# Performance work log

Hardware: AMD Instinct MI355X
Metric: run time of the kernel (lower is better)

## Reference

```python
import jax, jax.numpy as jnp
import numpy as np

D_MODEL = 1024
N_HEADS = 16
D_HEAD = D_MODEL // N_HEADS


def setup_inputs() -> dict:
    key = jax.random.key(0)
    ks = jax.random.split(key, 5)
    scale = 1.0 / np.sqrt(D_MODEL)
    return {
        "x": jax.random.normal(ks[0], (2, 2048, D_MODEL), dtype=jnp.float32),
        "W_q": jax.random.normal(ks[1], (D_MODEL, D_MODEL), dtype=jnp.float32) * scale,
        "W_k": jax.random.normal(ks[2], (D_MODEL, D_MODEL), dtype=jnp.float32) * scale,
        "W_v": jax.random.normal(ks[3], (D_MODEL, D_MODEL), dtype=jnp.float32) * scale,
        "W_o": jax.random.normal(ks[4], (D_MODEL, D_MODEL), dtype=jnp.float32) * scale,
    }


def reference(x, W_q, W_k, W_v, W_o):
    B, S, _ = x.shape
    # nn.Linear computes x @ W.T; weights stored [out, in]
    def proj(W):
        y = jnp.einsum("bsd,ed->bse", x, W)
        return y.reshape(B, S, N_HEADS, D_HEAD).transpose(0, 2, 1, 3)  # [B,H,S,Dh]

    q, k, v = proj(W_q), proj(W_k), proj(W_v)
    scores = jnp.einsum("bhqd,bhkd->bhqk", q, k) / jnp.sqrt(jnp.float32(D_HEAD))
    causal = jnp.triu(jnp.ones((S, S), dtype=bool), k=1)
    scores = jnp.where(causal, -jnp.inf, scores)
    attn = jax.nn.softmax(scores, axis=-1)
    out = jnp.einsum("bhqk,bhkd->bhqd", attn, v)  # [B,H,S,Dh]
    out = out.transpose(0, 2, 1, 3).reshape(B, S, D_MODEL)
    return jnp.einsum("bsd,ed->bse", out, W_o)
```

## Files before the change

kernel.cpp:

```cpp
#include <hip/hip_runtime.h>


#define DMODEL 1024
#define NHEADS 16
#define DHEAD  64
#define SEQ    2048
#define BATCH  2
#define MROWS  (BATCH * SEQ)

typedef __bf16 bf16x8 __attribute__((ext_vector_type(8)));
typedef __bf16 bf16x4 __attribute__((ext_vector_type(4)));
typedef float  f32x4  __attribute__((ext_vector_type(4)));

__device__ __forceinline__ f32x4 mfma16(bf16x8 a, bf16x8 b, f32x4 c) {
    return __builtin_amdgcn_mfma_f32_16x16x32_bf16(a, b, c, 0, 0, 0);
}

__device__ __forceinline__ bf16x8 ld8(const float* p) {
    const f32x4 a0 = *(const f32x4*)p;
    const f32x4 a1 = *(const f32x4*)(p + 4);
    bf16x8 v;
    v[0] = (__bf16)a0[0]; v[1] = (__bf16)a0[1];
    v[2] = (__bf16)a0[2]; v[3] = (__bf16)a0[3];
    v[4] = (__bf16)a1[0]; v[5] = (__bf16)a1[1];
    v[6] = (__bf16)a1[2]; v[7] = (__bf16)a1[3];
    return v;
}

__device__ __forceinline__ void gll16(const __bf16* g, __bf16* l) {
    __builtin_amdgcn_global_load_lds(
        (const __attribute__((address_space(1))) void*)g,
        (__attribute__((address_space(3))) void*)l,
        16, 0, 0);
}

__global__ __launch_bounds__(256) void cvt_kernel(const float* __restrict__ x,
                                                  const float* __restrict__ Wq,
                                                  const float* __restrict__ Wk,
                                                  const float* __restrict__ Wv,
                                                  const float* __restrict__ Wo,
                                                  __bf16* __restrict__ xb,
                                                  __bf16* __restrict__ wcat) {
    const int y = blockIdx.y;
    const float* src;
    __bf16* dst;
    int nchunks;
    if (y == 0) { src = x; dst = xb; nchunks = (MROWS * DMODEL) / 8; }
    else {
        src = (y == 1) ? Wq : (y == 2) ? Wk : (y == 3) ? Wv : Wo;
        dst = wcat + (size_t)(y - 1) * DMODEL * DMODEL;
        nchunks = (DMODEL * DMODEL) / 8;
    }
    const int c = blockIdx.x * 256 + threadIdx.x;
    if (c < nchunks) *(bf16x8*)(dst + (size_t)c * 8) = ld8(src + (size_t)c * 8);
}

template <typename TC>
__device__ __forceinline__ void gemm_bb_body(const __bf16* __restrict__ A,
                                             const __bf16* __restrict__ W,
                                             TC* __restrict__ C,
                                             int m0, int n0) {
    constexpr int K = DMODEL;
    __shared__ __align__(16) __bf16 As[128][32];
    __shared__ __align__(16) __bf16 Bs[128][32];

    const int tid  = threadIdx.x;
    const int lane = tid & 63;
    const int wave = tid >> 6;
    const int quad = lane >> 4;
    const int l16  = lane & 15;
    const int wm   = wave & 1;
    const int wn   = wave >> 1;

    const int srow = lane >> 2;
    const int scol = (lane & 3) * 8;

    const __bf16* a0p = A + (size_t)(m0 + wave * 16 + srow) * K + scol;
    const __bf16* a1p = A + (size_t)(m0 + 64 + wave * 16 + srow) * K + scol;
    const __bf16* b0p = W + (size_t)(n0 + wave * 16 + srow) * K + scol;
    const __bf16* b1p = W + (size_t)(n0 + 64 + wave * 16 + srow) * K + scol;

    f32x4 acc[4][4] = {};

    for (int k0 = 0; k0 < K; k0 += 32) {
        __syncthreads();
        gll16(a0p + k0, &As[wave * 16][0]);
        gll16(a1p + k0, &As[64 + wave * 16][0]);
        gll16(b0p + k0, &Bs[wave * 16][0]);
        gll16(b1p + k0, &Bs[64 + wave * 16][0]);
        __syncthreads();

        bf16x8 af[4], bfr[4];
#pragma unroll
        for (int i = 0; i < 4; ++i) {
            af[i]  = *(const bf16x8*)(&As[wm * 64 + i * 16 + l16][quad * 8]);
            bfr[i] = *(const bf16x8*)(&Bs[wn * 64 + i * 16 + l16][quad * 8]);
        }
#pragma unroll
        for (int mi = 0; mi < 4; ++mi)
#pragma unroll
            for (int ni = 0; ni < 4; ++ni)
                acc[mi][ni] = mfma16(af[mi], bfr[ni], acc[mi][ni]);
    }

#pragma unroll
    for (int mi = 0; mi < 4; ++mi)
#pragma unroll
        for (int ni = 0; ni < 4; ++ni)
#pragma unroll
            for (int r = 0; r < 4; ++r) {
                int row = m0 + wm * 64 + mi * 16 + quad * 4 + r;
                int col = n0 + wn * 64 + ni * 16 + l16;
                C[(size_t)row * DMODEL + col] = (TC)acc[mi][ni][r];
            }
}

__global__ __launch_bounds__(256) void qkv_kernel(const __bf16* __restrict__ X,
                                                  const __bf16* __restrict__ wcat,
                                                  __bf16* __restrict__ QKV) {
    const __bf16* W = wcat + (size_t)blockIdx.z * DMODEL * DMODEL;
    __bf16*       Y = QKV + (size_t)blockIdx.z * MROWS * DMODEL;
    gemm_bb_body<__bf16>(X, W, Y, blockIdx.y * 128, blockIdx.x * 128);
}

__global__ __launch_bounds__(256) void out_gemm_kernel(const __bf16* __restrict__ A,
                                                       const __bf16* __restrict__ W,
                                                       float* __restrict__ C) {
    gemm_bb_body<float>(A, W, C, blockIdx.y * 128, blockIdx.x * 128);
}

__global__ __launch_bounds__(128) void attn_kernel(const __bf16* __restrict__ Q,
                                                   const __bf16* __restrict__ Kg,
                                                   const __bf16* __restrict__ Vg,
                                                   __bf16* __restrict__ O) {
    const int pr = blockIdx.x;
    const int bh = blockIdx.y;
    const int b = bh >> 4, h = bh & 15;
    const size_t base = (size_t)b * SEQ * DMODEL + (size_t)h * DHEAD;

    const int tid  = threadIdx.x;
    const int lane = tid & 63;
    const int wave = tid >> 6;
    const int quad = lane >> 4;
    const int l16  = lane & 15;

    __shared__ __align__(16) __bf16 Ks[32][80];
    __shared__ __align__(16) __bf16 Vt[64][40];
    __shared__ __align__(16) __bf16 Ps[2][16][40];

    const int ldr = tid >> 2;
    const int c0  = (tid & 3) * 16;
    const int vcol = (((ldr >> 3) ^ (c0 >> 4)) << 3) | (ldr & 7);

#pragma unroll
    for (int sel = 0; sel < 2; ++sel) {
        const int qt = sel ? (63 - pr) : pr;
        const int qrow = qt * 32 + wave * 16 + l16;

        const bf16x8 qf0 = *(const bf16x8*)(Q + base + (size_t)qrow * DMODEL + quad * 8);
        const bf16x8 qf1 = *(const bf16x8*)(Q + base + (size_t)qrow * DMODEL + 32 + quad * 8);

        f32x4 oacc[4] = {};
        float m_i = -1e30f, l_i = 0.f;

        const int ktiles = qt + 1;

        const __bf16* kp = Kg + base + (size_t)ldr * DMODEL + c0;
        const __bf16* vp = Vg + base + (size_t)ldr * DMODEL + c0;
        bf16x8 pk0 = *(const bf16x8*)(kp);
        bf16x8 pk1 = *(const bf16x8*)(kp + 8);
        bf16x8 pv0 = *(const bf16x8*)(vp);
        bf16x8 pv1 = *(const bf16x8*)(vp + 8);

        for (int kt = 0; kt < ktiles; ++kt) {
            *(bf16x8*)(&Ks[ldr][c0])     = pk0;
            *(bf16x8*)(&Ks[ldr][c0 + 8]) = pk1;
#pragma unroll
            for (int i = 0; i < 8; ++i) {
                Vt[c0 + i][vcol]     = pv0[i];
                Vt[c0 + 8 + i][vcol] = pv1[i];
            }
            __syncthreads();

            if (kt + 1 < ktiles) {
                const __bf16* kp2 = Kg + base + (size_t)((kt + 1) * 32 + ldr) * DMODEL + c0;
                const __bf16* vp2 = Vg + base + (size_t)((kt + 1) * 32 + ldr) * DMODEL + c0;
                pk0 = *(const bf16x8*)(kp2);
                pk1 = *(const bf16x8*)(kp2 + 8);
                pv0 = *(const bf16x8*)(vp2);
                pv1 = *(const bf16x8*)(vp2 + 8);
            }

            const int k0 = kt * 32;

            const bf16x8 kf00 = *(const bf16x8*)(&Ks[l16][quad * 8]);
            const bf16x8 kf01 = *(const bf16x8*)(&Ks[l16][32 + quad * 8]);
            const bf16x8 kf10 = *(const bf16x8*)(&Ks[16 + l16][quad * 8]);
            const bf16x8 kf11 = *(const bf16x8*)(&Ks[16 + l16][32 + quad * 8]);
            f32x4 s0 = {}, s1 = {};
            s0 = mfma16(kf00, qf0, s0); s0 = mfma16(kf01, qf1, s0);
            s1 = mfma16(kf10, qf0, s1); s1 = mfma16(kf11, qf1, s1);

            float sc[2][4];
            bool  ok[2][4];
            float mx = -1e30f;
#pragma unroll
            for (int hh = 0; hh < 2; ++hh)
#pragma unroll
                for (int r = 0; r < 4; ++r) {
                    const int kk = k0 + hh * 16 + quad * 4 + r;
                    const float v = (hh ? s1[r] : s0[r]) * 0.125f;
                    sc[hh][r] = v;
                    ok[hh][r] = (kk <= qrow);
                    mx = fmaxf(mx, ok[hh][r] ? v : -1e30f);
                }
            mx = fmaxf(mx, __shfl_xor(mx, 16));
            mx = fmaxf(mx, __shfl_xor(mx, 32));
            const float mnew  = fmaxf(m_i, mx);
            const float alpha = __expf(m_i - mnew);
            m_i = mnew;

            float p[2][4];
            float rs = 0.f;
#pragma unroll
            for (int hh = 0; hh < 2; ++hh)
#pragma unroll
                for (int r = 0; r < 4; ++r) {
                    p[hh][r] = ok[hh][r] ? __expf(sc[hh][r] - mnew) : 0.f;
                    rs += p[hh][r];
                }
            rs += __shfl_xor(rs, 16);
            rs += __shfl_xor(rs, 32);
            l_i = l_i * alpha + rs;

            bf16x4 w0, w1;
#pragma unroll
            for (int r = 0; r < 4; ++r) { w0[r] = (__bf16)p[0][r]; w1[r] = (__bf16)p[1][r]; }
            *(bf16x4*)(&Ps[wave][l16][quad * 4])      = w0;
            *(bf16x4*)(&Ps[wave][l16][16 + quad * 4]) = w1;

            const bf16x8 pf = *(const bf16x8*)(&Ps[wave][l16][quad * 8]);
#pragma unroll
            for (int f = 0; f < 4; ++f) {
                const bf16x8 vf = *(const bf16x8*)(&Vt[f * 16 + l16][(quad ^ f) * 8]);
                oacc[f] = mfma16(vf, pf, oacc[f] * alpha);
            }
            __syncthreads();
        }

        const float inv = (l_i > 0.f) ? (1.f / l_i) : 0.f;
#pragma unroll
        for (int f = 0; f < 4; ++f) {
            bf16x4 o;
#pragma unroll
            for (int r = 0; r < 4; ++r) o[r] = (__bf16)(oacc[f][r] * inv);
            *(bf16x4*)(O + base + (size_t)qrow * DMODEL + f * 16 + quad * 4) = o;
        }
    }
}

extern "C" void kernel_launch(void* const* d_in, const int* in_sizes, int n_in,
                              void* d_out, int out_size, void* d_ws, size_t ws_size,
                              hipStream_t stream) {
    const float* x  = (const float*)d_in[0];
    const float* Wq = (const float*)d_in[1];
    const float* Wk = (const float*)d_in[2];
    const float* Wv = (const float*)d_in[3];
    const float* Wo = (const float*)d_in[4];
    float* out = (float*)d_out;

    const size_t tm = (size_t)MROWS * DMODEL;
    const size_t tw = (size_t)DMODEL * DMODEL;
    __bf16* xb   = (__bf16*)d_ws;
    __bf16* wcat = xb + tm;
    __bf16* QKV  = wcat + 4 * tw;
    __bf16* Q = QKV;
    __bf16* K = QKV + tm;
    __bf16* V = QKV + 2 * tm;

    dim3 gc(2048, 5);
    cvt_kernel<<<gc, 256, 0, stream>>>(x, Wq, Wk, Wv, Wo, xb, wcat);

    dim3 g1(DMODEL / 128, MROWS / 128, 3);
    qkv_kernel<<<g1, 256, 0, stream>>>(xb, wcat, QKV);

    dim3 g2(SEQ / 64, BATCH * NHEADS);
    attn_kernel<<<g2, 128, 0, stream>>>(Q, K, V, Q);

    dim3 g3(DMODEL / 128, MROWS / 128);
    out_gemm_kernel<<<g3, 256, 0, stream>>>(Q, wcat + 3 * tw, out);
}
```

Baseline: 220.7 us.

## Fold softmax scale into Q projection, use exp2, split attention per q-tile

The Q projection epilogue now multiplies by 0.125*log2(e), so the attention kernel can drop the per-score multiply and use exp2f directly. Causal masking is applied only on the diagonal tile, so off-diagonal tiles skip the compare and select work. The paired q-tile scheme, where one block handled tile pr and tile 63-pr, is replaced by one q-tile per block with twice as many blocks, launched heaviest-first. This adds parallelism and frees the loop from the outer sel iteration, but may unbalance per-block work. Rounding Q to bf16 after scaling slightly changes numerics.

```diff
diff --git a/kernel.cpp b/kernel.cpp
--- a/kernel.cpp
+++ b/kernel.cpp
@@ -59,7 +59,7 @@
 __device__ __forceinline__ void gemm_bb_body(const __bf16* __restrict__ A,
                                              const __bf16* __restrict__ W,
                                              TC* __restrict__ C,
-                                             int m0, int n0) {
+                                             int m0, int n0, float scale) {
     constexpr int K = DMODEL;
     __shared__ __align__(16) __bf16 As[128][32];
     __shared__ __align__(16) __bf16 Bs[128][32];
@@ -111,29 +111,32 @@
             for (int r = 0; r < 4; ++r) {
                 int row = m0 + wm * 64 + mi * 16 + quad * 4 + r;
                 int col = n0 + wn * 64 + ni * 16 + l16;
-                C[(size_t)row * DMODEL + col] = (TC)acc[mi][ni][r];
+                C[(size_t)row * DMODEL + col] = (TC)(acc[mi][ni][r] * scale);
             }
 }
+
+#define QSCALE 0.1803368801111204f
 
 __global__ __launch_bounds__(256) void qkv_kernel(const __bf16* __restrict__ X,
                                                   const __bf16* __restrict__ wcat,
                                                   __bf16* __restrict__ QKV) {
     const __bf16* W = wcat + (size_t)blockIdx.z * DMODEL * DMODEL;
     __bf16*       Y = QKV + (size_t)blockIdx.z * MROWS * DMODEL;
-    gemm_bb_body<__bf16>(X, W, Y, blockIdx.y * 128, blockIdx.x * 128);
+    const float scale = (blockIdx.z == 0) ? QSCALE : 1.0f;
+    gemm_bb_body<__bf16>(X, W, Y, blockIdx.y * 128, blockIdx.x * 128, scale);
 }
 
 __global__ __launch_bounds__(256) void out_gemm_kernel(const __bf16* __restrict__ A,
                                                        const __bf16* __restrict__ W,
                                                        float* __restrict__ C) {
-    gemm_bb_body<float>(A, W, C, blockIdx.y * 128, blockIdx.x * 128);
+    gemm_bb_body<float>(A, W, C, blockIdx.y * 128, blockIdx.x * 128, 1.0f);
 }
 
 __global__ __launch_bounds__(128) void attn_kernel(const __bf16* __restrict__ Q,
                                                    const __bf16* __restrict__ Kg,
                                                    const __bf16* __restrict__ Vg,
                                                    __bf16* __restrict__ O) {
-    const int pr = blockIdx.x;
+    const int qt = 63 - blockIdx.x;
     const int bh = blockIdx.y;
     const int b = bh >> 4, h = bh & 15;
     const size_t base = (size_t)b * SEQ * DMODEL + (size_t)h * DHEAD;
@@ -152,110 +155,123 @@
     const int c0  = (tid & 3) * 16;
     const int vcol = (((ldr >> 3) ^ (c0 >> 4)) << 3) | (ldr & 7);
 
-#pragma unroll
-    for (int sel = 0; sel < 2; ++sel) {
-        const int qt = sel ? (63 - pr) : pr;
-        const int qrow = qt * 32 + wave * 16 + l16;
-
-        const bf16x8 qf0 = *(const bf16x8*)(Q + base + (size_t)qrow * DMODEL + quad * 8);
-        const bf16x8 qf1 = *(const bf16x8*)(Q + base + (size_t)qrow * DMODEL + 32 + quad * 8);
-
-        f32x4 oacc[4] = {};
-        float m_i = -1e30f, l_i = 0.f;
-
-        const int ktiles = qt + 1;
-
-        const __bf16* kp = Kg + base + (size_t)ldr * DMODEL + c0;
-        const __bf16* vp = Vg + base + (size_t)ldr * DMODEL + c0;
-        bf16x8 pk0 = *(const bf16x8*)(kp);
-        bf16x8 pk1 = *(const bf16x8*)(kp + 8);
-        bf16x8 pv0 = *(const bf16x8*)(vp);
-        bf16x8 pv1 = *(const bf16x8*)(vp + 8);
-
-        for (int kt = 0; kt < ktiles; ++kt) {
-            *(bf16x8*)(&Ks[ldr][c0])     = pk0;
-            *(bf16x8*)(&Ks[ldr][c0 + 8]) = pk1;
-#pragma unroll
-            for (int i = 0; i < 8; ++i) {
-                Vt[c0 + i][vcol]     = pv0[i];
-                Vt[c0 + 8 + i][vcol] = pv1[i];
-            }
-            __syncthreads();
-
-            if (kt + 1 < ktiles) {
-                const __bf16* kp2 = Kg + base + (size_t)((kt + 1) * 32 + ldr) * DMODEL + c0;
-                const __bf16* vp2 = Vg + base + (size_t)((kt + 1) * 32 + ldr) * DMODEL + c0;
-                pk0 = *(const bf16x8*)(kp2);
-                pk1 = *(const bf16x8*)(kp2 + 8);
-                pv0 = *(const bf16x8*)(vp2);
-                pv1 = *(const bf16x8*)(vp2 + 8);
-            }
-
-            const int k0 = kt * 32;
-
-            const bf16x8 kf00 = *(const bf16x8*)(&Ks[l16][quad * 8]);
-            const bf16x8 kf01 = *(const bf16x8*)(&Ks[l16][32 + quad * 8]);
-            const bf16x8 kf10 = *(const bf16x8*)(&Ks[16 + l16][quad * 8]);
-            const bf16x8 kf11 = *(const bf16x8*)(&Ks[16 + l16][32 + quad * 8]);
-            f32x4 s0 = {}, s1 = {};
-            s0 = mfma16(kf00, qf0, s0); s0 = mfma16(kf01, qf1, s0);
-            s1 = mfma16(kf10, qf0, s1); s1 = mfma16(kf11, qf1, s1);
-
-            float sc[2][4];
-            bool  ok[2][4];
-            float mx = -1e30f;
+    const int qrow = qt * 32 + wave * 16 + l16;
+
+    const bf16x8 qf0 = *(const bf16x8*)(Q + base + (size_t)qrow * DMODEL + quad * 8);
+    const bf16x8 qf1 = *(const bf16x8*)(Q + base + (size_t)qrow * DMODEL + 32 + quad * 8);
+
+    f32x4 oacc[4] = {};
+    float m_i = -1e30f, l_i = 0.f;
+
+    const __bf16* kp = Kg + base + (size_t)ldr * DMODEL + c0;
+    const __bf16* vp = Vg + base + (size_t)ldr * DMODEL + c0;
+    bf16x8 pk0 = *(const bf16x8*)(kp);
+    bf16x8 pk1 = *(const bf16x8*)(kp + 8);
+    bf16x8 pv0 = *(const bf16x8*)(vp);
+    bf16x8 pv1 = *(const bf16x8*)(vp + 8);
+
+    for (int kt = 0; kt <= qt; ++kt) {
+        *(bf16x8*)(&Ks[ldr][c0])     = pk0;
+        *(bf16x8*)(&Ks[ldr][c0 + 8]) = pk1;
+#pragma unroll
+        for (int i = 0; i < 8; ++i) {
+            Vt[c0 + i][vcol]     = pv0[i];
+            Vt[c0 + 8 + i][vcol] = pv1[i];
+        }
+        __syncthreads();
+
+        if (kt < qt) {
+            const __bf16* kp2 = Kg + base + (size_t)((kt + 1) * 32 + ldr) * DMODEL + c0;
+            const __bf16* vp2 = Vg + base + (size_t)((kt + 1) * 32 + ldr) * DMODEL + c0;
+            pk0 = *(const bf16x8*)(kp2);
+            pk1 = *(const bf16x8*)(kp2 + 8);
+            pv0 = *(const bf16x8*)(vp2);
+            pv1 = *(const bf16x8*)(vp2 + 8);
+        }
+
+        const int k0 = kt * 32;
+        const bool diag = (kt == qt);
+
+        const bf16x8 kf00 = *(const bf16x8*)(&Ks[l16][quad * 8]);
+        const bf16x8 kf01 = *(const bf16x8*)(&Ks[l16][32 + quad * 8]);
+        const bf16x8 kf10 = *(const bf16x8*)(&Ks[16 + l16][quad * 8]);
+        const bf16x8 kf11 = *(const bf16x8*)(&Ks[16 + l16][32 + quad * 8]);
+        f32x4 s0 = {}, s1 = {};
+        s0 = mfma16(kf00, qf0, s0); s0 = mfma16(kf01, qf1, s0);
+        s1 = mfma16(kf10, qf0, s1); s1 = mfma16(kf11, qf1, s1);
+
+        float mx;
+        bool ok[2][4];
+        if (!diag) {
+            float m0 = s0[0];
+#pragma unroll
+            for (int r = 1; r < 4; ++r) m0 = fmaxf(m0, s0[r]);
+#pragma unroll
+            for (int r = 0; r < 4; ++r) m0 = fmaxf(m0, s1[r]);
+            mx = m0;
+        } else {
+            mx = -1e30f;
 #pragma unroll
             for (int hh = 0; hh < 2; ++hh)
 #pragma unroll
                 for (int r = 0; r < 4; ++r) {
                     const int kk = k0 + hh * 16 + quad * 4 + r;
-                    const float v = (hh ? s1[r] : s0[r]) * 0.125f;
-                    sc[hh][r] = v;
                     ok[hh][r] = (kk <= qrow);
+                    const float v = hh ? s1[r] : s0[r];
                     mx = fmaxf(mx, ok[hh][r] ? v : -1e30f);
                 }
-            mx = fmaxf(mx, __shfl_xor(mx, 16));
-            mx = fmaxf(mx, __shfl_xor(mx, 32));
-            const float mnew  = fmaxf(m_i, mx);
-            const float alpha = __expf(m_i - mnew);
-            m_i = mnew;
-
-            float p[2][4];
-            float rs = 0.f;
+        }
+        mx = fmaxf(mx, __shfl_xor(mx, 16));
+        mx = fmaxf(mx, __shfl_xor(mx, 32));
+        const float mnew  = fmaxf(m_i, mx);
+        const float alpha = exp2f(m_i - mnew);
+        m_i = mnew;
+
+        float p[2][4];
+        float rs = 0.f;
+        if (!diag) {
 #pragma unroll
             for (int hh = 0; hh < 2; ++hh)
 #pragma unroll
                 for (int r = 0; r < 4; ++r) {
-                    p[hh][r] = ok[hh][r] ? __expf(sc[hh][r] - mnew) : 0.f;
+                    p[hh][r] = exp2f((hh ? s1[r] : s0[r]) - mnew);
                     rs += p[hh][r];
                 }
-            rs += __shfl_xor(rs, 16);
-            rs += __shfl_xor(rs, 32);
-            l_i = l_i * alpha + rs;
-
-            bf16x4 w0, w1;
-#pragma unroll
-            for (int r = 0; r < 4; ++r) { w0[r] = (__bf16)p[0][r]; w1[r] = (__bf16)p[1][r]; }
-            *(bf16x4*)(&Ps[wave][l16][quad * 4])      = w0;
-            *(bf16x4*)(&Ps[wave][l16][16 + quad * 4]) = w1;
-
-            const bf16x8 pf = *(const bf16x8*)(&Ps[wave][l16][quad * 8]);
-#pragma unroll
-            for (int f = 0; f < 4; ++f) {
-                const bf16x8 vf = *(const bf16x8*)(&Vt[f * 16 + l16][(quad ^ f) * 8]);
-                oacc[f] = mfma16(vf, pf, oacc[f] * alpha);
-            }
-            __syncthreads();
-        }
-
-        const float inv = (l_i > 0.f) ? (1.f / l_i) : 0.f;
+        } else {
+#pragma unroll
+            for (int hh = 0; hh < 2; ++hh)
+#pragma unroll
+                for (int r = 0; r < 4; ++r) {
+                    p[hh][r] = ok[hh][r] ? exp2f((hh ? s1[r] : s0[r]) - mnew) : 0.f;
+                    rs += p[hh][r];
+                }
+        }
+        rs += __shfl_xor(rs, 16);
+        rs += __shfl_xor(rs, 32);
+        l_i = l_i * alpha + rs;
+
+        bf16x4 w0, w1;
+#pragma unroll
+        for (int r = 0; r < 4; ++r) { w0[r] = (__bf16)p[0][r]; w1[r] = (__bf16)p[1][r]; }
+        *(bf16x4*)(&Ps[wave][l16][quad * 4])      = w0;
+        *(bf16x4*)(&Ps[wave][l16][16 + quad * 4]) = w1;
+
+        const bf16x8 pf = *(const bf16x8*)(&Ps[wave][l16][quad * 8]);
 #pragma unroll
         for (int f = 0; f < 4; ++f) {
-            bf16x4 o;
-#pragma unroll
-            for (int r = 0; r < 4; ++r) o[r] = (__bf16)(oacc[f][r] * inv);
-            *(bf16x4*)(O + base + (size_t)qrow * DMODEL + f * 16 + quad * 4) = o;
-        }
+            const bf16x8 vf = *(const bf16x8*)(&Vt[f * 16 + l16][(quad ^ f) * 8]);
+            oacc[f] = mfma16(vf, pf, oacc[f] * alpha);
+        }
+        __syncthreads();
+    }
+
+    const float inv = (l_i > 0.f) ? (1.f / l_i) : 0.f;
+#pragma unroll
+    for (int f = 0; f < 4; ++f) {
+        bf16x4 o;
+#pragma unroll
+        for (int r = 0; r < 4; ++r) o[r] = (__bf16)(oacc[f][r] * inv);
+        *(bf16x4*)(O + base + (size_t)qrow * DMODEL + f * 16 + quad * 4) = o;
     }
 }
 
@@ -284,7 +300,7 @@
     dim3 g1(DMODEL / 128, MROWS / 128, 3);
     qkv_kernel<<<g1, 256, 0, stream>>>(xb, wcat, QKV);
 
-    dim3 g2(SEQ / 64, BATCH * NHEADS);
+    dim3 g2(SEQ / 32, BATCH * NHEADS);
     attn_kernel<<<g2, 128, 0, stream>>>(Q, K, V, Q);
 
     dim3 g3(DMODEL / 128, MROWS / 128);
```

Result: slower. 247.2 us (+12.0%).
